# Optimization experiments

Hardware: AMD Instinct MI355X
Metric: run time of the kernel (lower is better)

The kernel has to match this reference:

```python
import jax, jax.numpy as jnp
import numpy as np

B, S, D_IN, D_OUT, R = 4, 1024, 1024, 1024, 8

def setup_inputs() -> dict:
    key = jax.random.key(0)
    k1, k2, k3, k4, k5 = jax.random.split(key, 5)
    scale = 1.0 / np.sqrt(D_IN)
    return {
        "x": jax.random.normal(k1, (B, S, D_IN), dtype=jnp.float32),
        "A_params": jax.random.normal(k2, (B, S, D_OUT, R), dtype=jnp.float32) * 0.02,
        "B_params": jax.random.normal(k3, (B, S, R, D_IN), dtype=jnp.float32) * 0.02,
        "W": jax.random.normal(k4, (D_OUT, D_IN), dtype=jnp.float32) * scale,
        "b": jax.random.normal(k5, (D_OUT,), dtype=jnp.float32) * scale,
    }

def reference(x, A_params, B_params, W, b):
    # base linear: y = x @ W^T + b  -> [B, S, D_OUT]
    base_out = jnp.einsum('bsi,oi->bso', x, W) + b
    # per-token low-rank update: (x @ B^T) @ A^T
    inter = jnp.einsum('bsi,bsri->bsr', x, B_params)           # [B, S, R]
    adaptation = jnp.einsum('bsr,bsor->bso', inter, A_params)  # [B, S, D_OUT]
    return base_out + adaptation
```

## Files before the change

### kernel.cpp

```cpp
#include <hip/hip_runtime.h>
#include <hip/hip_bf16.h>
#include <stdint.h>

#define TOKENS 4096
#define DIN 1024
#define DOUT 1024
#define RANK 8

typedef __attribute__((ext_vector_type(4))) float f32x4;
typedef __attribute__((ext_vector_type(8))) short short8;

__device__ __forceinline__ unsigned short f2bf(float f) {
    union { float f; unsigned u; } v; v.f = f;
    unsigned r = v.u + 0x7FFFu + ((v.u >> 16) & 1u);
    return (unsigned short)(r >> 16);
}

__global__ __launch_bounds__(256) void k_convert_w(const float* __restrict__ W,
                                                   ushort* __restrict__ Wb) {
    int i = blockIdx.x * 256 + threadIdx.x;
    float4 v = ((const float4*)W)[i];
    ushort4 u;
    u.x = f2bf(v.x); u.y = f2bf(v.y); u.z = f2bf(v.z); u.w = f2bf(v.w);
    ((ushort4*)Wb)[i] = u;
}

__global__ __launch_bounds__(256) void k_inter(const float* __restrict__ x,
                                               const float* __restrict__ Bp,
                                               float* __restrict__ inter,
                                               ushort* __restrict__ xb) {
    int t = blockIdx.x;
    int tid = threadIdx.x;
    int lane = tid & 63, wave = tid >> 6;

    const float4* x4 = (const float4*)(x + (size_t)t * DIN);
    float4 xv = x4[tid];

    ushort4 u;
    u.x = f2bf(xv.x); u.y = f2bf(xv.y); u.z = f2bf(xv.z); u.w = f2bf(xv.w);
    ((ushort4*)(xb + (size_t)t * DIN))[tid] = u;

    const float4* B4 = (const float4*)(Bp + (size_t)t * RANK * DIN);
    float acc[RANK];
#pragma unroll
    for (int r = 0; r < RANK; ++r) {
        float4 bv = B4[r * 256 + tid];
        acc[r] = xv.x * bv.x + xv.y * bv.y + xv.z * bv.z + xv.w * bv.w;
    }

    __shared__ float part[4][RANK];
#pragma unroll
    for (int r = 0; r < RANK; ++r) {
        float v = acc[r];
#pragma unroll
        for (int off = 32; off > 0; off >>= 1) v += __shfl_xor(v, off, 64);
        if (lane == 0) part[wave][r] = v;
    }
    __syncthreads();
    if (tid < RANK) {
        float s = part[0][tid] + part[1][tid] + part[2][tid] + part[3][tid];
        inter[(size_t)t * RANK + tid] = s;
    }
}

__global__ __launch_bounds__(256) void k_gemm(const ushort* __restrict__ Xb,
                                              const ushort* __restrict__ Wb,
                                              const float* __restrict__ bias,
                                              const float* __restrict__ inter,
                                              const float* __restrict__ Ap,
                                              float* __restrict__ out) {
    __shared__ ushort As[64 * 64];
    __shared__ ushort Bs[128 * 64];

    const int tid = threadIdx.x;
    const int lane = tid & 63, wave = tid >> 6;
    const int M0 = blockIdx.x * 64;
    const int N0 = blockIdx.y * 128;
    const int col16 = lane & 15;
    const int kg = lane >> 4;

    f32x4 acc[4][2] = {};

    for (int kt = 0; kt < DIN; kt += 64) {
        __syncthreads();
#pragma unroll
        for (int it = 0; it < 2; ++it) {
            int flat = it * 256 + tid;
            int row = flat >> 3, ch = flat & 7;
            const ushort* g = Xb + (size_t)(M0 + row) * DIN + kt + ch * 8;
            __builtin_amdgcn_global_load_lds(
                (const __attribute__((address_space(1))) void*)g,
                (__attribute__((address_space(3))) void*)(As + flat * 8), 16, 0, 0);
        }
#pragma unroll
        for (int it = 0; it < 4; ++it) {
            int flat = it * 256 + tid;
            int row = flat >> 3, ch = flat & 7;
            const ushort* g = Wb + (size_t)(N0 + row) * DIN + kt + ch * 8;
            __builtin_amdgcn_global_load_lds(
                (const __attribute__((address_space(1))) void*)g,
                (__attribute__((address_space(3))) void*)(Bs + flat * 8), 16, 0, 0);
        }
        asm volatile("s_waitcnt vmcnt(0)" ::: "memory");
        __syncthreads();

#pragma unroll
        for (int ks = 0; ks < 2; ++ks) {
            short8 a[4], b[2];
#pragma unroll
            for (int mf = 0; mf < 4; ++mf)
                a[mf] = *(const short8*)(As + (mf * 16 + col16) * 64 + ks * 32 + kg * 8);
#pragma unroll
            for (int nf = 0; nf < 2; ++nf)
                b[nf] = *(const short8*)(Bs + (wave * 32 + nf * 16 + col16) * 64 + ks * 32 + kg * 8);
#pragma unroll
            for (int mf = 0; mf < 4; ++mf)
#pragma unroll
                for (int nf = 0; nf < 2; ++nf)
                    acc[mf][nf] = __builtin_amdgcn_mfma_f32_16x16x32_bf16(
                        a[mf], b[nf], acc[mf][nf], 0, 0, 0);
        }
    }

#pragma unroll
    for (int nf = 0; nf < 2; ++nf) {
        int o = N0 + wave * 32 + nf * 16 + col16;
        float bb = bias[o];
#pragma unroll
        for (int mf = 0; mf < 4; ++mf) {
#pragma unroll
            for (int rg = 0; rg < 4; ++rg) {
                int m = M0 + mf * 16 + kg * 4 + rg;
                const float4* a8 = (const float4*)(Ap + ((size_t)m * DOUT + o) * RANK);
                const float4* iv = (const float4*)(inter + (size_t)m * RANK);
                float4 a0 = a8[0], a1 = a8[1];
                float4 i0 = iv[0], i1 = iv[1];
                float ad = a0.x * i0.x + a0.y * i0.y + a0.z * i0.z + a0.w * i0.w +
                           a1.x * i1.x + a1.y * i1.y + a1.z * i1.z + a1.w * i1.w;
                out[(size_t)m * DOUT + o] = acc[mf][nf][rg] + bb + ad;
            }
        }
    }
}

extern "C" void kernel_launch(void* const* d_in, const int* in_sizes, int n_in,
                              void* d_out, int out_size, void* d_ws, size_t ws_size,
                              hipStream_t stream) {
    const float* x    = (const float*)d_in[0];
    const float* Ap   = (const float*)d_in[1];
    const float* Bp   = (const float*)d_in[2];
    const float* W    = (const float*)d_in[3];
    const float* bias = (const float*)d_in[4];
    float* out = (float*)d_out;

    ushort* xb = (ushort*)d_ws;
    ushort* Wb = xb + (size_t)TOKENS * DIN;
    float* inter = (float*)(Wb + (size_t)DOUT * DIN);

    hipLaunchKernelGGL(k_convert_w, dim3(DOUT * DIN / 1024), dim3(256), 0, stream, W, Wb);
    hipLaunchKernelGGL(k_inter, dim3(TOKENS), dim3(256), 0, stream, x, Bp, inter, xb);
    hipLaunchKernelGGL(k_gemm, dim3(TOKENS / 64, DOUT / 128), dim3(256), 0, stream,
                       xb, Wb, bias, inter, Ap, out);
}
```

Measured before the change: 84.39 us.

## Move LoRA adaptation and bias into per-token kernel, GEMM accumulates into output

The low-rank adaptation and bias are now computed in the per-token kernel, which reads A_params with fully coalesced float4 loads and writes the partial output directly. This removes the strided per-element A_params gathers from the GEMM epilogue and drops the intermediate buffer. The GEMM now does a read-modify-write on the output, which adds an extra 16MB read of out. Its tiling also changes to 128x64 tiles in a 2x2 wave layout, and the grid is reordered so that blocks next to each other share an X tile.

```diff
diff --git a/kernel.cpp b/kernel.cpp
--- a/kernel.cpp
+++ b/kernel.cpp
@@ -25,16 +25,17 @@
     ((ushort4*)Wb)[i] = u;
 }
 
-__global__ __launch_bounds__(256) void k_inter(const float* __restrict__ x,
-                                               const float* __restrict__ Bp,
-                                               float* __restrict__ inter,
-                                               ushort* __restrict__ xb) {
-    int t = blockIdx.x;
-    int tid = threadIdx.x;
-    int lane = tid & 63, wave = tid >> 6;
+__global__ __launch_bounds__(256) void k_lora(const float* __restrict__ x,
+                                              const float* __restrict__ Bp,
+                                              const float* __restrict__ Ap,
+                                              const float* __restrict__ bias,
+                                              float* __restrict__ out,
+                                              ushort* __restrict__ xb) {
+    const int t = blockIdx.x;
+    const int tid = threadIdx.x;
+    const int lane = tid & 63, wave = tid >> 6;
 
-    const float4* x4 = (const float4*)(x + (size_t)t * DIN);
-    float4 xv = x4[tid];
+    float4 xv = ((const float4*)(x + (size_t)t * DIN))[tid];
 
     ushort4 u;
     u.x = f2bf(xv.x); u.y = f2bf(xv.y); u.z = f2bf(xv.z); u.w = f2bf(xv.w);
@@ -49,6 +50,7 @@
     }
 
     __shared__ float part[4][RANK];
+    __shared__ float sint[RANK];
 #pragma unroll
     for (int r = 0; r < RANK; ++r) {
         float v = acc[r];
@@ -57,25 +59,39 @@
         if (lane == 0) part[wave][r] = v;
     }
     __syncthreads();
-    if (tid < RANK) {
-        float s = part[0][tid] + part[1][tid] + part[2][tid] + part[3][tid];
-        inter[(size_t)t * RANK + tid] = s;
+    if (tid < RANK)
+        sint[tid] = part[0][tid] + part[1][tid] + part[2][tid] + part[3][tid];
+    __syncthreads();
+
+    const float i0 = sint[0], i1 = sint[1], i2 = sint[2], i3 = sint[3];
+    const float i4 = sint[4], i5 = sint[5], i6 = sint[6], i7 = sint[7];
+
+    const float4* A4 = (const float4*)(Ap + ((size_t)t * DOUT + tid * 4) * RANK);
+    float res[4];
+#pragma unroll
+    for (int j = 0; j < 4; ++j) {
+        float4 a0 = A4[j * 2], a1 = A4[j * 2 + 1];
+        res[j] = a0.x * i0 + a0.y * i1 + a0.z * i2 + a0.w * i3 +
+                 a1.x * i4 + a1.y * i5 + a1.z * i6 + a1.w * i7;
     }
+    float4 bb = ((const float4*)bias)[tid];
+    float4 o4;
+    o4.x = res[0] + bb.x; o4.y = res[1] + bb.y;
+    o4.z = res[2] + bb.z; o4.w = res[3] + bb.w;
+    ((float4*)(out + (size_t)t * DOUT))[tid] = o4;
 }
 
-__global__ __launch_bounds__(256) void k_gemm(const ushort* __restrict__ Xb,
-                                              const ushort* __restrict__ Wb,
-                                              const float* __restrict__ bias,
-                                              const float* __restrict__ inter,
-                                              const float* __restrict__ Ap,
-                                              float* __restrict__ out) {
-    __shared__ ushort As[64 * 64];
-    __shared__ ushort Bs[128 * 64];
+__global__ __launch_bounds__(256) void k_gemm_add(const ushort* __restrict__ Xb,
+                                                  const ushort* __restrict__ Wb,
+                                                  float* __restrict__ out) {
+    __shared__ ushort As[128 * 64];
+    __shared__ ushort Bs[64 * 64];
 
     const int tid = threadIdx.x;
     const int lane = tid & 63, wave = tid >> 6;
-    const int M0 = blockIdx.x * 64;
-    const int N0 = blockIdx.y * 128;
+    const int wm = wave >> 1, wn = wave & 1;
+    const int M0 = blockIdx.y * 128;
+    const int N0 = blockIdx.x * 64;
     const int col16 = lane & 15;
     const int kg = lane >> 4;
 
@@ -84,7 +100,7 @@
     for (int kt = 0; kt < DIN; kt += 64) {
         __syncthreads();
 #pragma unroll
-        for (int it = 0; it < 2; ++it) {
+        for (int it = 0; it < 4; ++it) {
             int flat = it * 256 + tid;
             int row = flat >> 3, ch = flat & 7;
             const ushort* g = Xb + (size_t)(M0 + row) * DIN + kt + ch * 8;
@@ -93,7 +109,7 @@
                 (__attribute__((address_space(3))) void*)(As + flat * 8), 16, 0, 0);
         }
 #pragma unroll
-        for (int it = 0; it < 4; ++it) {
+        for (int it = 0; it < 2; ++it) {
             int flat = it * 256 + tid;
             int row = flat >> 3, ch = flat & 7;
             const ushort* g = Wb + (size_t)(N0 + row) * DIN + kt + ch * 8;
@@ -109,10 +125,10 @@
             short8 a[4], b[2];
 #pragma unroll
             for (int mf = 0; mf < 4; ++mf)
-                a[mf] = *(const short8*)(As + (mf * 16 + col16) * 64 + ks * 32 + kg * 8);
+                a[mf] = *(const short8*)(As + (wm * 64 + mf * 16 + col16) * 64 + ks * 32 + kg * 8);
 #pragma unroll
             for (int nf = 0; nf < 2; ++nf)
-                b[nf] = *(const short8*)(Bs + (wave * 32 + nf * 16 + col16) * 64 + ks * 32 + kg * 8);
+                b[nf] = *(const short8*)(Bs + (wn * 32 + nf * 16 + col16) * 64 + ks * 32 + kg * 8);
 #pragma unroll
             for (int mf = 0; mf < 4; ++mf)
 #pragma unroll
@@ -124,20 +140,14 @@
 
 #pragma unroll
     for (int nf = 0; nf < 2; ++nf) {
-        int o = N0 + wave * 32 + nf * 16 + col16;
-        float bb = bias[o];
+        int o = N0 + wn * 32 + nf * 16 + col16;
 #pragma unroll
         for (int mf = 0; mf < 4; ++mf) {
 #pragma unroll
             for (int rg = 0; rg < 4; ++rg) {
-                int m = M0 + mf * 16 + kg * 4 + rg;
-                const float4* a8 = (const float4*)(Ap + ((size_t)m * DOUT + o) * RANK);
-                const float4* iv = (const float4*)(inter + (size_t)m * RANK);
-                float4 a0 = a8[0], a1 = a8[1];
-                float4 i0 = iv[0], i1 = iv[1];
-                float ad = a0.x * i0.x + a0.y * i0.y + a0.z * i0.z + a0.w * i0.w +
-                           a1.x * i1.x + a1.y * i1.y + a1.z * i1.z + a1.w * i1.w;
-                out[(size_t)m * DOUT + o] = acc[mf][nf][rg] + bb + ad;
+                int m = M0 + wm * 64 + mf * 16 + kg * 4 + rg;
+                size_t idx = (size_t)m * DOUT + o;
+                out[idx] += acc[mf][nf][rg];
             }
         }
     }
@@ -155,10 +165,10 @@
 
     ushort* xb = (ushort*)d_ws;
     ushort* Wb = xb + (size_t)TOKENS * DIN;
-    float* inter = (float*)(Wb + (size_t)DOUT * DIN);
 
     hipLaunchKernelGGL(k_convert_w, dim3(DOUT * DIN / 1024), dim3(256), 0, stream, W, Wb);
-    hipLaunchKernelGGL(k_inter, dim3(TOKENS), dim3(256), 0, stream, x, Bp, inter, xb);
-    hipLaunchKernelGGL(k_gemm, dim3(TOKENS / 64, DOUT / 128), dim3(256), 0, stream,
-                       xb, Wb, bias, inter, Ap, out);
+    hipLaunchKernelGGL(k_lora, dim3(TOKENS), dim3(256), 0, stream,
+                       x, Bp, Ap, bias, out, xb);
+    hipLaunchKernelGGL(k_gemm_add, dim3(DOUT / 64, TOKENS / 128), dim3(256), 0, stream,
+                       xb, Wb, out);
 }
```

New measurement: 82.61 us. 1.02x faster.

## Fuse low-rank projection, x conversion and GEMM into one per-token-block kernel

Applied to the files above, without the earlier changes.

The separate intermediate kernel and the tiled GEMM are replaced by one kernel that handles 8 tokens per block. Each block converts x to bf16 into swizzled LDS, padded to 16 rows with zeros, and computes the rank-8 intermediates in shared memory. It then runs the MFMA GEMM over all 1024 outputs, reading bf16 W directly from global memory or cache. This removes the xb and inter round trips through global memory and one launch. In exchange, half of each MFMA tile is zero padding, and every block re-reads the whole of W without LDS staging, which puts heavy pressure on L2 bandwidth.

```diff
diff --git a/kernel.cpp b/kernel.cpp
--- a/kernel.cpp
+++ b/kernel.cpp
@@ -6,6 +6,7 @@
 #define DIN 1024
 #define DOUT 1024
 #define RANK 8
+#define TPB 8
 
 typedef __attribute__((ext_vector_type(4))) float f32x4;
 typedef __attribute__((ext_vector_type(8))) short short8;
@@ -14,6 +15,10 @@
     union { float f; unsigned u; } v; v.f = f;
     unsigned r = v.u + 0x7FFFu + ((v.u >> 16) & 1u);
     return (unsigned short)(r >> 16);
+}
+
+__device__ __forceinline__ float dot4(float4 a, float4 b) {
+    return a.x * b.x + a.y * b.y + a.z * b.z + a.w * b.w;
 }
 
 __global__ __launch_bounds__(256) void k_convert_w(const float* __restrict__ W,
@@ -25,119 +30,93 @@
     ((ushort4*)Wb)[i] = u;
 }
 
-__global__ __launch_bounds__(256) void k_inter(const float* __restrict__ x,
+__global__ __launch_bounds__(256) void k_fused(const float* __restrict__ x,
                                                const float* __restrict__ Bp,
-                                               float* __restrict__ inter,
-                                               ushort* __restrict__ xb) {
-    int t = blockIdx.x;
-    int tid = threadIdx.x;
-    int lane = tid & 63, wave = tid >> 6;
-
-    const float4* x4 = (const float4*)(x + (size_t)t * DIN);
-    float4 xv = x4[tid];
-
-    ushort4 u;
-    u.x = f2bf(xv.x); u.y = f2bf(xv.y); u.z = f2bf(xv.z); u.w = f2bf(xv.w);
-    ((ushort4*)(xb + (size_t)t * DIN))[tid] = u;
-
-    const float4* B4 = (const float4*)(Bp + (size_t)t * RANK * DIN);
-    float acc[RANK];
-#pragma unroll
-    for (int r = 0; r < RANK; ++r) {
-        float4 bv = B4[r * 256 + tid];
-        acc[r] = xv.x * bv.x + xv.y * bv.y + xv.z * bv.z + xv.w * bv.w;
-    }
-
-    __shared__ float part[4][RANK];
-#pragma unroll
-    for (int r = 0; r < RANK; ++r) {
-        float v = acc[r];
-#pragma unroll
-        for (int off = 32; off > 0; off >>= 1) v += __shfl_xor(v, off, 64);
-        if (lane == 0) part[wave][r] = v;
-    }
-    __syncthreads();
-    if (tid < RANK) {
-        float s = part[0][tid] + part[1][tid] + part[2][tid] + part[3][tid];
-        inter[(size_t)t * RANK + tid] = s;
-    }
-}
-
-__global__ __launch_bounds__(256) void k_gemm(const ushort* __restrict__ Xb,
-                                              const ushort* __restrict__ Wb,
-                                              const float* __restrict__ bias,
-                                              const float* __restrict__ inter,
-                                              const float* __restrict__ Ap,
-                                              float* __restrict__ out) {
-    __shared__ ushort As[64 * 64];
-    __shared__ ushort Bs[128 * 64];
+                                               const float* __restrict__ Ap,
+                                               const ushort* __restrict__ Wb,
+                                               const float* __restrict__ bias,
+                                               float* __restrict__ out) {
+    __shared__ ushort xls[16 * DIN];
+    __shared__ float sInter[TPB * RANK];
 
     const int tid = threadIdx.x;
-    const int lane = tid & 63, wave = tid >> 6;
-    const int M0 = blockIdx.x * 64;
-    const int N0 = blockIdx.y * 128;
-    const int col16 = lane & 15;
-    const int kg = lane >> 4;
+    const int lane = tid & 63, wid = tid >> 6;
+    const int col16 = lane & 15, kg = lane >> 4;
+    const int T0 = blockIdx.x * TPB;
 
-    f32x4 acc[4][2] = {};
-
-    for (int kt = 0; kt < DIN; kt += 64) {
-        __syncthreads();
+    float4 xv[2][4];
 #pragma unroll
-        for (int it = 0; it < 2; ++it) {
-            int flat = it * 256 + tid;
-            int row = flat >> 3, ch = flat & 7;
-            const ushort* g = Xb + (size_t)(M0 + row) * DIN + kt + ch * 8;
-            __builtin_amdgcn_global_load_lds(
-                (const __attribute__((address_space(1))) void*)g,
-                (__attribute__((address_space(3))) void*)(As + flat * 8), 16, 0, 0);
+    for (int tt = 0; tt < 2; ++tt) {
+        const int tl = wid * 2 + tt;
+        const float4* xp = (const float4*)(x + (size_t)(T0 + tl) * DIN);
+#pragma unroll
+        for (int j = 0; j < 4; ++j) {
+            float4 v = xp[j * 64 + lane];
+            xv[tt][j] = v;
+            ushort4 u;
+            u.x = f2bf(v.x); u.y = f2bf(v.y); u.z = f2bf(v.z); u.w = f2bf(v.w);
+            const int c = (lane >> 1) + j * 32;
+            const int cs = c ^ (tl & 7);
+            *(ushort4*)((char*)xls + tl * 2048 + cs * 16 + (lane & 1) * 8) = u;
         }
+    }
 #pragma unroll
-        for (int it = 0; it < 4; ++it) {
-            int flat = it * 256 + tid;
-            int row = flat >> 3, ch = flat & 7;
-            const ushort* g = Wb + (size_t)(N0 + row) * DIN + kt + ch * 8;
-            __builtin_amdgcn_global_load_lds(
-                (const __attribute__((address_space(1))) void*)g,
-                (__attribute__((address_space(3))) void*)(Bs + flat * 8), 16, 0, 0);
-        }
-        asm volatile("s_waitcnt vmcnt(0)" ::: "memory");
-        __syncthreads();
-
+    for (int tt = 0; tt < 2; ++tt) {
+        const int rp = 8 + wid * 2 + tt;
+        ushort4 z = {0, 0, 0, 0};
 #pragma unroll
-        for (int ks = 0; ks < 2; ++ks) {
-            short8 a[4], b[2];
-#pragma unroll
-            for (int mf = 0; mf < 4; ++mf)
-                a[mf] = *(const short8*)(As + (mf * 16 + col16) * 64 + ks * 32 + kg * 8);
-#pragma unroll
-            for (int nf = 0; nf < 2; ++nf)
-                b[nf] = *(const short8*)(Bs + (wave * 32 + nf * 16 + col16) * 64 + ks * 32 + kg * 8);
-#pragma unroll
-            for (int mf = 0; mf < 4; ++mf)
-#pragma unroll
-                for (int nf = 0; nf < 2; ++nf)
-                    acc[mf][nf] = __builtin_amdgcn_mfma_f32_16x16x32_bf16(
-                        a[mf], b[nf], acc[mf][nf], 0, 0, 0);
-        }
+        for (int j = 0; j < 4; ++j)
+            *(ushort4*)((char*)xls + rp * 2048 + (j * 64 + lane) * 8) = z;
     }
 
 #pragma unroll
-    for (int nf = 0; nf < 2; ++nf) {
-        int o = N0 + wave * 32 + nf * 16 + col16;
-        float bb = bias[o];
+    for (int tt = 0; tt < 2; ++tt) {
+        const int tl = wid * 2 + tt;
+        const float4* bp = (const float4*)(Bp + (size_t)(T0 + tl) * RANK * DIN);
 #pragma unroll
-        for (int mf = 0; mf < 4; ++mf) {
+        for (int r = 0; r < RANK; ++r) {
+            float s = 0.f;
 #pragma unroll
-            for (int rg = 0; rg < 4; ++rg) {
-                int m = M0 + mf * 16 + kg * 4 + rg;
-                const float4* a8 = (const float4*)(Ap + ((size_t)m * DOUT + o) * RANK);
-                const float4* iv = (const float4*)(inter + (size_t)m * RANK);
-                float4 a0 = a8[0], a1 = a8[1];
-                float4 i0 = iv[0], i1 = iv[1];
-                float ad = a0.x * i0.x + a0.y * i0.y + a0.z * i0.z + a0.w * i0.w +
-                           a1.x * i1.x + a1.y * i1.y + a1.z * i1.z + a1.w * i1.w;
-                out[(size_t)m * DOUT + o] = acc[mf][nf][rg] + bb + ad;
+            for (int j = 0; j < 4; ++j)
+                s += dot4(bp[r * 256 + j * 64 + lane], xv[tt][j]);
+#pragma unroll
+            for (int off = 32; off > 0; off >>= 1)
+                s += __shfl_xor(s, off, 64);
+            if (lane == 0) sInter[tl * RANK + r] = s;
+        }
+    }
+    __syncthreads();
+
+#pragma unroll
+    for (int ps = 0; ps < 4; ++ps) {
+        const int ob = ps * 256 + wid * 64;
+        f32x4 acc[4] = {};
+#pragma unroll
+        for (int ks = 0; ks < 32; ++ks) {
+            const int cs = (ks * 4 + kg) ^ (col16 & 7);
+            short8 af = *(const short8*)(xls + col16 * DIN + cs * 8);
+#pragma unroll
+            for (int nf = 0; nf < 4; ++nf) {
+                short8 bf = *(const short8*)(Wb + (size_t)(ob + nf * 16 + col16) * DIN +
+                                             ks * 32 + kg * 8);
+                acc[nf] = __builtin_amdgcn_mfma_f32_16x16x32_bf16(af, bf, acc[nf], 0, 0, 0);
+            }
+        }
+        if (kg < 2) {
+#pragma unroll
+            for (int nf = 0; nf < 4; ++nf) {
+                const int o = ob + nf * 16 + col16;
+                const float bb = bias[o];
+#pragma unroll
+                for (int rg = 0; rg < 4; ++rg) {
+                    const int tl = kg * 4 + rg;
+                    const float4* ap = (const float4*)(Ap + ((size_t)(T0 + tl) * DOUT + o) * RANK);
+                    float4 a0 = ap[0], a1 = ap[1];
+                    const float4* iv = (const float4*)(sInter + tl * RANK);
+                    float4 i0 = iv[0], i1 = iv[1];
+                    float d = dot4(a0, i0) + dot4(a1, i1);
+                    out[(size_t)(T0 + tl) * DOUT + o] = acc[nf][rg] + bb + d;
+                }
             }
         }
     }
@@ -153,12 +132,9 @@
     const float* bias = (const float*)d_in[4];
     float* out = (float*)d_out;
 
-    ushort* xb = (ushort*)d_ws;
-    ushort* Wb = xb + (size_t)TOKENS * DIN;
-    float* inter = (float*)(Wb + (size_t)DOUT * DIN);
+    ushort* Wb = (ushort*)d_ws;
 
     hipLaunchKernelGGL(k_convert_w, dim3(DOUT * DIN / 1024), dim3(256), 0, stream, W, Wb);
-    hipLaunchKernelGGL(k_inter, dim3(TOKENS), dim3(256), 0, stream, x, Bp, inter, xb);
-    hipLaunchKernelGGL(k_gemm, dim3(TOKENS / 64, DOUT / 128), dim3(256), 0, stream,
-                       xb, Wb, bias, inter, Ap, out);
+    hipLaunchKernelGGL(k_fused, dim3(TOKENS / TPB), dim3(256), 0, stream,
+                       x, Bp, Ap, Wb, bias, out);
 }
```

Result: slower. 199.3 us (+136.2%).
